# Kernel tuning notes

Measured on AMD Instinct MI355X. Metric: run time of the kernel, lower is better.

The kernel has to match this reference:

```python
import jax, jax.numpy as jnp
import numpy as np

N = 4096          # nodes (= Mamba sequence length)
E_EDGES = 65536   # edges
D = 512           # dim_h (= d_inner, expand=1)
NEXP = 4          # num_experts (cfg.model.num_experts)
DSTATE = 16
DCONV = 4
DTRANK = 32       # ceil(D/16)
EPS = 1e-5


def _silu(x):
    return x * jax.nn.sigmoid(x)


def _bn(h, g, b):
    # BatchNorm1d over node axis (batch statistics)
    mu = h.mean(0)
    var = h.var(0)
    return (h - mu) * jax.lax.rsqrt(var + EPS) * g + b


def _mamba(u, in_w, conv_w, conv_b, x_w, dt_w, dt_b, A_log, Dp, out_w):
    # u: [L, D] single-sequence Mamba(d_model=D, d_state=16, d_conv=4, expand=1)
    L = u.shape[0]
    xz = u @ in_w                      # [L, 2D]
    xc, z = xz[:, :D], xz[:, D:]
    xp = jnp.pad(xc, ((DCONV - 1, 0), (0, 0)))
    xconv = conv_b
    for k in range(DCONV):             # depthwise causal conv, tiny fixed loop
        xconv = xconv + conv_w[:, k] * xp[k:k + L]
    xs = _silu(xconv)                  # [L, D]
    dbc = xs @ x_w                     # [L, DTRANK + 2*DSTATE]
    dt = jax.nn.softplus(dbc[:, :DTRANK] @ dt_w + dt_b)          # [L, D]
    Bm = dbc[:, DTRANK:DTRANK + DSTATE]                          # [L, S]
    Cm = dbc[:, DTRANK + DSTATE:]                                # [L, S]
    A = -jnp.exp(A_log)                                          # [D, S]
    dA = jnp.exp(dt[:, :, None] * A[None])                       # [L, D, S]
    dBu = dt[:, :, None] * Bm[:, None, :] * xs[:, :, None]       # [L, D, S]

    def step(hprev, inp):
        dA_t, dBu_t, C_t = inp
        hn = dA_t * hprev + dBu_t
        return hn, (hn * C_t[None, :]).sum(-1)

    _, ys = jax.lax.scan(step, jnp.zeros((D, DSTATE), u.dtype), (dA, dBu, Cm))
    y = ys + Dp * xs
    return (y * _silu(z)) @ out_w      # [L, D]


def setup_inputs() -> dict:
    key = jax.random.key(0)
    ks = jax.random.split(key, 24)
    s = 1.0 / np.sqrt(D)
    inp = {}
    inp['x'] = jax.random.normal(ks[0], (N, D), jnp.float32)
    inp['edge_index'] = jax.random.randint(ks[1], (2, E_EDGES), 0, N)
    inp['edge_attr'] = jax.random.normal(ks[2], (E_EDGES, D), jnp.float32)
    # GINE nn: Linear(D,D) -> ReLU -> Linear(D,D)
    inp['gin_w1'] = jax.random.normal(ks[3], (D, D)) * s
    inp['gin_b1'] = jnp.zeros((D,))
    inp['gin_w2'] = jax.random.normal(ks[4], (D, D)) * s
    inp['gin_b2'] = jnp.zeros((D,))
    # BatchNorms
    inp['bn1l_g'] = jnp.ones((D,)); inp['bn1l_b'] = jnp.zeros((D,))
    inp['bn1a_g'] = jnp.ones((D,)); inp['bn1a_b'] = jnp.zeros((D,))
    inp['bn2_g'] = jnp.ones((D,)); inp['bn2_b'] = jnp.zeros((D,))
    # gating MLP [D, D//2, NEXP]
    inp['gate_w1'] = jax.random.normal(ks[5], (D, D // 2)) * s
    inp['gate_b1'] = jnp.zeros((D // 2,))
    inp['gate_w2'] = jax.random.normal(ks[6], (D // 2, NEXP)) * (1.0 / np.sqrt(D // 2))
    inp['gate_b2'] = jnp.zeros((NEXP,))
    # stacked per-expert Mamba params
    inp['in_w'] = jax.random.normal(ks[7], (NEXP, D, 2 * D)) * s
    inp['conv_w'] = jax.random.normal(ks[8], (NEXP, D, DCONV)) * 0.5
    inp['conv_b'] = jnp.zeros((NEXP, D))
    inp['x_w'] = jax.random.normal(ks[9], (NEXP, D, DTRANK + 2 * DSTATE)) * s
    inp['dt_w'] = jax.random.normal(ks[10], (NEXP, DTRANK, D)) * (1.0 / np.sqrt(DTRANK))
    inp['dt_b'] = jax.random.normal(ks[11], (NEXP, D)) * 0.1 - 4.0
    A0 = jnp.log(jnp.arange(1, DSTATE + 1, dtype=jnp.float32))
    inp['A_log'] = jnp.broadcast_to(A0, (NEXP, D, DSTATE)).copy()
    inp['Dp'] = jnp.ones((NEXP, D))
    inp['out_w'] = jax.random.normal(ks[12], (NEXP, D, D)) * s
    # FFN
    inp['ff_w1'] = jax.random.normal(ks[13], (D, 2 * D)) * s
    inp['ff_b1'] = jnp.zeros((2 * D,))
    inp['ff_w2'] = jax.random.normal(ks[14], (2 * D, D)) * (1.0 / np.sqrt(2 * D))
    inp['ff_b2'] = jnp.zeros((D,))
    return inp


def reference(x, edge_index, edge_attr,
              gin_w1, gin_b1, gin_w2, gin_b2,
              bn1l_g, bn1l_b, bn1a_g, bn1a_b, bn2_g, bn2_b,
              gate_w1, gate_b1, gate_w2, gate_b2,
              in_w, conv_w, conv_b, x_w, dt_w, dt_b, A_log, Dp, out_w,
              ff_w1, ff_b1, ff_w2, ff_b2):
    h_in = x
    src, dst = edge_index[0], edge_index[1]
    # local GINEConv: nn(x + sum_j relu(x_j + e_ji))
    msg = jax.nn.relu(x[src] + edge_attr)                      # [E, D]
    aggr = jax.ops.segment_sum(msg, dst, num_segments=N)       # [N, D]
    h_local = jax.nn.relu((x + aggr) @ gin_w1 + gin_b1) @ gin_w2 + gin_b2
    h_local = _bn(h_in + h_local, bn1l_g, bn1l_b)
    # gated mixture of Mamba experts
    gate = jax.nn.softmax(jax.nn.relu(x @ gate_w1 + gate_b1) @ gate_w2 + gate_b2, axis=-1)  # [N, NEXP]
    ys = jax.vmap(_mamba, in_axes=(None, 0, 0, 0, 0, 0, 0, 0, 0, 0))(
        x, in_w, conv_w, conv_b, x_w, dt_w, dt_b, A_log, Dp, out_w)  # [NEXP, N, D]
    h_attn = jnp.einsum('ne,end->nd', gate, ys)
    h_attn = _bn(h_in + h_attn, bn1a_g, bn1a_b)
    # fuse + FFN
    h = h_local + h_attn
    ff = jax.nn.relu(h @ ff_w1 + ff_b1) @ ff_w2 + ff_b2
    return _bn(h + ff, bn2_g, bn2_b)
```

## Files before the change

### kernel.cpp

```cpp
#include <hip/hip_runtime.h>
#include <hip/hip_bf16.h>
#include <math.h>

#define N_NODES 4096
#define E_EDGE 65536
#define D 512
#define NEXP 4
#define DSTATE 16
#define DCONV 4
#define DTRANK 32
#define EPS 1e-5f
#define LCHUNK 32
#define NCHUNK (N_NODES / LCHUNK)

typedef __hip_bfloat16 bf16;
typedef short bf16x8 __attribute__((ext_vector_type(8)));
typedef float f32x4 __attribute__((ext_vector_type(4)));

__device__ __forceinline__ float siluf(float x) { return x / (1.f + __expf(-x)); }
__device__ __forceinline__ float softplusf(float x) {
  return (x > 20.f) ? x : log1pf(__expf(x));
}

__device__ __forceinline__ void gload16(const void* g, void* l) {
  __builtin_amdgcn_global_load_lds(
      (const __attribute__((address_space(1))) void*)g,
      (__attribute__((address_space(3))) void*)l, 16, 0, 0);
}

template <int FN, int EPI>
__global__ __launch_bounds__(256, 2) void mm_k(
    const bf16* __restrict__ A, int lda, long sA,
    const bf16* __restrict__ Bt, int ldb, long sB,
    const float* __restrict__ bias,
    float* __restrict__ Cf, bf16* __restrict__ Cb, int ldc, long sC, int K) {
  constexpr int BN = FN * 32;
  __shared__ __align__(16) bf16 As[128 * 32];
  __shared__ __align__(16) bf16 Bs[BN * 32];
  const int z = blockIdx.z;
  A += (size_t)z * sA;
  Bt += (size_t)z * sB;
  const int tid = threadIdx.x;
  const int w = tid >> 6, l = tid & 63;
  const int wr = w >> 1, wc = w & 1;
  const int bm = blockIdx.y * 128, bn = blockIdx.x * BN;

  f32x4 acc[4][FN];
#pragma unroll
  for (int i = 0; i < 4; ++i)
#pragma unroll
    for (int j = 0; j < FN; ++j) acc[i][j] = 0.f;

  const int srow = l >> 2, schunk = l & 3;
  const bf16* gA = A + (size_t)(bm + w * 16 + srow) * lda + schunk * 8;
  const bf16* gB = Bt + (size_t)(bn + w * 16 + srow) * ldb + schunk * 8;
  bf16* lA = As + w * 512;
  bf16* lB = Bs + w * 512;

  const int ar = wr * 64 + (l & 15);
  const int br = wc * FN * 16 + (l & 15);
  const int kb = l >> 4;

  for (int k0 = 0; k0 < K; k0 += 32) {
    gload16(gA + k0, lA);
    gload16(gA + k0 + (size_t)64 * lda, lA + 64 * 32);
    gload16(gB + k0, lB);
    if (FN == 4) gload16(gB + k0 + (size_t)64 * ldb, lB + 64 * 32);
    __syncthreads();
    const bf16x8* Ap = (const bf16x8*)As;
    const bf16x8* Bp = (const bf16x8*)Bs;
    bf16x8 af[4], bfr[FN];
#pragma unroll
    for (int i = 0; i < 4; ++i) af[i] = Ap[(ar + i * 16) * 4 + kb];
#pragma unroll
    for (int j = 0; j < FN; ++j) bfr[j] = Bp[(br + j * 16) * 4 + kb];
#pragma unroll
    for (int i = 0; i < 4; ++i)
#pragma unroll
      for (int j = 0; j < FN; ++j)
        acc[i][j] = __builtin_amdgcn_mfma_f32_16x16x32_bf16(af[i], bfr[j], acc[i][j], 0, 0, 0);
    __syncthreads();
  }

  if (Cf) Cf += (size_t)z * sC;
  if (Cb) Cb += (size_t)z * sC;
  const int r0 = bm + wr * 64 + (l >> 4) * 4;
  const int c0 = bn + wc * FN * 16 + (l & 15);
#pragma unroll
  for (int i = 0; i < 4; ++i)
#pragma unroll
    for (int j = 0; j < FN; ++j) {
      const int col = c0 + j * 16;
      const float bv = bias ? bias[col] : 0.f;
#pragma unroll
      for (int r = 0; r < 4; ++r) {
        const int row = r0 + i * 16 + r;
        float v = acc[i][j][r] + bv;
        if (EPI == 1) v = fmaxf(v, 0.f);
        if (Cf) Cf[(size_t)row * ldc + col] = v;
        if (Cb) Cb[(size_t)row * ldc + col] = __float2bfloat16(v);
      }
    }
}

__global__ __launch_bounds__(256) void wtrans_k(const float* __restrict__ in,
                                                bf16* __restrict__ out, int K, int N,
                                                int ldo, long s_in, long s_out) {
  __shared__ float t[32][33];
  in += (size_t)blockIdx.z * s_in;
  out += (size_t)blockIdx.z * s_out;
  const int n0 = blockIdx.x * 32, k0 = blockIdx.y * 32;
  const int tx = threadIdx.x & 31, ty = threadIdx.x >> 5;
  for (int i = ty; i < 32; i += 8) t[i][tx] = in[(size_t)(k0 + i) * N + n0 + tx];
  __syncthreads();
  for (int i = ty; i < 32; i += 8)
    out[(size_t)(n0 + i) * ldo + k0 + tx] = __float2bfloat16(t[tx][i]);
}

__global__ void hist_k(const int* __restrict__ ei, int* __restrict__ deg) {
  int e = blockIdx.x * 256 + threadIdx.x;
  if (e < E_EDGE) atomicAdd(&deg[ei[E_EDGE + e]], 1);
}

__global__ __launch_bounds__(1024) void prefix_k(const int* __restrict__ deg,
                                                 int* __restrict__ rowstart) {
  __shared__ int s[1024];
  int t = threadIdx.x;
  int base = t * 4;
  int d0 = deg[base], d1 = deg[base + 1], d2 = deg[base + 2], d3 = deg[base + 3];
  int sum = d0 + d1 + d2 + d3;
  s[t] = sum;
  __syncthreads();
  for (int off = 1; off < 1024; off <<= 1) {
    int v = (t >= off) ? s[t - off] : 0;
    __syncthreads();
    s[t] += v;
    __syncthreads();
  }
  int excl = s[t] - sum;
  rowstart[base] = excl;
  rowstart[base + 1] = excl + d0;
  rowstart[base + 2] = excl + d0 + d1;
  rowstart[base + 3] = excl + d0 + d1 + d2;
}

__global__ void scatter_k(const int* __restrict__ ei, const int* __restrict__ rowstart,
                          int* __restrict__ cnt, int* __restrict__ eid) {
  int e = blockIdx.x * 256 + threadIdx.x;
  if (e < E_EDGE) {
    int dst = ei[E_EDGE + e];
    int slot = rowstart[dst] + atomicAdd(&cnt[dst], 1);
    eid[slot] = e;
  }
}

__global__ __launch_bounds__(256) void aggr_gather_k(
    const float* __restrict__ x, const int* __restrict__ ei, const float* __restrict__ ea,
    const int* __restrict__ rowstart, const int* __restrict__ deg,
    const int* __restrict__ eid, bf16* __restrict__ hpre, bf16* __restrict__ xbf) {
  int n = blockIdx.x;
  int tid = threadIdx.x;
  int beg = rowstart[n];
  int end = beg + deg[n];
  float a0 = 0.f, a1 = 0.f;
  int i = beg;
  for (; i + 1 < end; i += 2) {
    int e0 = eid[i], e1 = eid[i + 1];
    int s0 = ei[e0], s1 = ei[e1];
    const float* x0 = x + (size_t)s0 * D;
    const float* e0p = ea + (size_t)e0 * D;
    const float* x1 = x + (size_t)s1 * D;
    const float* e1p = ea + (size_t)e1 * D;
    a0 += fmaxf(x0[tid] + e0p[tid], 0.f) + fmaxf(x1[tid] + e1p[tid], 0.f);
    a1 += fmaxf(x0[tid + 256] + e0p[tid + 256], 0.f) +
          fmaxf(x1[tid + 256] + e1p[tid + 256], 0.f);
  }
  if (i < end) {
    int e0 = eid[i];
    int s0 = ei[e0];
    const float* x0 = x + (size_t)s0 * D;
    const float* e0p = ea + (size_t)e0 * D;
    a0 += fmaxf(x0[tid] + e0p[tid], 0.f);
    a1 += fmaxf(x0[tid + 256] + e0p[tid + 256], 0.f);
  }
  float xv0 = x[(size_t)n * D + tid];
  float xv1 = x[(size_t)n * D + tid + 256];
  hpre[(size_t)n * D + tid] = __float2bfloat16(xv0 + a0);
  hpre[(size_t)n * D + tid + 256] = __float2bfloat16(xv1 + a1);
  xbf[(size_t)n * D + tid] = __float2bfloat16(xv0);
  xbf[(size_t)n * D + tid + 256] = __float2bfloat16(xv1);
}

__global__ __launch_bounds__(256) void gate2_k(const float* __restrict__ g1,
                                               const float* __restrict__ w2,
                                               const float* __restrict__ b2,
                                               float* __restrict__ gate) {
  int row = blockIdx.x * 4 + (threadIdx.x >> 6);
  int lane = threadIdx.x & 63;
  float a0 = 0.f, a1 = 0.f, a2 = 0.f, a3 = 0.f;
  for (int k = lane; k < 256; k += 64) {
    float v = g1[(size_t)row * 256 + k];
    a0 = fmaf(v, w2[k * 4 + 0], a0);
    a1 = fmaf(v, w2[k * 4 + 1], a1);
    a2 = fmaf(v, w2[k * 4 + 2], a2);
    a3 = fmaf(v, w2[k * 4 + 3], a3);
  }
#pragma unroll
  for (int off = 32; off; off >>= 1) {
    a0 += __shfl_down(a0, off);
    a1 += __shfl_down(a1, off);
    a2 += __shfl_down(a2, off);
    a3 += __shfl_down(a3, off);
  }
  if (lane == 0) {
    float l0 = a0 + b2[0], l1 = a1 + b2[1], l2 = a2 + b2[2], l3 = a3 + b2[3];
    float m = fmaxf(fmaxf(l0, l1), fmaxf(l2, l3));
    float e0 = __expf(l0 - m), e1 = __expf(l1 - m), e2 = __expf(l2 - m), e3 = __expf(l3 - m);
    float s = 1.f / (e0 + e1 + e2 + e3);
    gate[row * 4 + 0] = e0 * s;
    gate[row * 4 + 1] = e1 * s;
    gate[row * 4 + 2] = e2 * s;
    gate[row * 4 + 3] = e3 * s;
  }
}

__global__ void conv_silu_k(const bf16* __restrict__ xz, const float* __restrict__ cw,
                            const float* __restrict__ cb, bf16* __restrict__ xs, int e0) {
  const int z = blockIdx.y;
  xz += (size_t)z * N_NODES * 2 * D;
  xs += (size_t)z * N_NODES * D;
  cw += (size_t)(e0 + z) * D * DCONV;
  cb += (size_t)(e0 + z) * D;
  int idx = blockIdx.x * blockDim.x + threadIdx.x;
  if (idx >= N_NODES * D) return;
  int t = idx >> 9;
  int d = idx & (D - 1);
  float acc = cb[d];
#pragma unroll
  for (int k = 0; k < DCONV; ++k) {
    int tt = t + k - (DCONV - 1);
    if (tt >= 0)
      acc = fmaf(cw[d * DCONV + k], __bfloat162float(xz[(size_t)tt * (2 * D) + d]), acc);
  }
  xs[idx] = __float2bfloat16(siluf(acc));
}

__global__ void dt_k(const float* __restrict__ dbc, const float* __restrict__ dtw,
                     const float* __restrict__ dtbias, bf16* __restrict__ dt, int e0) {
  const int z = blockIdx.y;
  dbc += (size_t)z * N_NODES * 64;
  dt += (size_t)z * N_NODES * D;
  dtw += (size_t)(e0 + z) * DTRANK * D;
  dtbias += (size_t)(e0 + z) * D;
  int idx = blockIdx.x * blockDim.x + threadIdx.x;
  int t = idx >> 9, d = idx & (D - 1);
  float acc = dtbias[d];
#pragma unroll
  for (int k = 0; k < DTRANK; ++k) acc = fmaf(dbc[t * 64 + k], dtw[k * D + d], acc);
  dt[idx] = __float2bfloat16(softplusf(acc));
}

__global__ __launch_bounds__(256) void colstats_k(const float* __restrict__ p,
                                                  const float* __restrict__ q,
                                                  float* __restrict__ acc) {
  __shared__ float sb[4][512], sb2[4][512];
  const int w = threadIdx.x >> 6, l = threadIdx.x & 63;
  float s[8], s2[8];
#pragma unroll
  for (int i = 0; i < 8; ++i) { s[i] = 0.f; s2[i] = 0.f; }
  for (int j = 0; j < 16; ++j) {
    size_t base = ((size_t)blockIdx.x * 64 + w * 16 + j) * D;
#pragma unroll
    for (int i = 0; i < 8; ++i) {
      int c = i * 64 + l;
      float v = p[base + c] + q[base + c];
      s[i] += v;
      s2[i] = fmaf(v, v, s2[i]);
    }
  }
#pragma unroll
  for (int i = 0; i < 8; ++i) {
    sb[w][i * 64 + l] = s[i];
    sb2[w][i * 64 + l] = s2[i];
  }
  __syncthreads();
  for (int c = threadIdx.x; c < 512; c += 256) {
    atomicAdd(&acc[c], sb[0][c] + sb[1][c] + sb[2][c] + sb[3][c]);
    atomicAdd(&acc[512 + c], sb2[0][c] + sb2[1][c] + sb2[2][c] + sb2[3][c]);
  }
}

__device__ __forceinline__ void bn_params(const float* acc, int d, float& mu, float& rsig) {
  mu = acc[d] * (1.f / N_NODES);
  float var = acc[512 + d] * (1.f / N_NODES) - mu * mu;
  rsig = rsqrtf(var + EPS);
}

__global__ void norm_k(const float* __restrict__ p, const float* __restrict__ q,
                       const float* __restrict__ acc, const float* __restrict__ g,
                       const float* __restrict__ b, float* __restrict__ o) {
  int idx = blockIdx.x * blockDim.x + threadIdx.x;
  if (idx >= N_NODES * D) return;
  int d = idx & (D - 1);
  float mu, rsig;
  bn_params(acc, d, mu, rsig);
  o[idx] = (p[idx] + q[idx] - mu) * rsig * g[d] + b[d];
}

__global__ void bnadd_k(const float* __restrict__ x, const float* __restrict__ hraw,
                        const float* __restrict__ acc, const float* __restrict__ g,
                        const float* __restrict__ b, const float* __restrict__ hloc,
                        float* __restrict__ of, bf16* __restrict__ ob) {
  int idx = blockIdx.x * blockDim.x + threadIdx.x;
  if (idx >= N_NODES * D) return;
  int d = idx & (D - 1);
  float mu, rsig;
  bn_params(acc, d, mu, rsig);
  float v = hloc[idx] + (x[idx] + hraw[idx] - mu) * rsig * g[d] + b[d];
  of[idx] = v;
  ob[idx] = __float2bfloat16(v);
}

__global__ __launch_bounds__(512) void scanA_k(const bf16* __restrict__ dt,
                                               const bf16* __restrict__ xs,
                                               const float* __restrict__ dbc,
                                               const float* __restrict__ Alog,
                                               float* __restrict__ Q,
                                               float* __restrict__ dtsum, int e0) {
  const int z = blockIdx.y;
  dt += (size_t)z * N_NODES * D;
  xs += (size_t)z * N_NODES * D;
  dbc += (size_t)z * N_NODES * 64;
  Alog += (size_t)(e0 + z) * D * DSTATE;
  Q += (size_t)z * NCHUNK * D * DSTATE;
  dtsum += (size_t)z * NCHUNK * D;
  int c = blockIdx.x;
  int d = threadIdx.x;
  float As[DSTATE], h[DSTATE];
#pragma unroll
  for (int s = 0; s < DSTATE; ++s) {
    As[s] = -__expf(Alog[d * DSTATE + s]);
    h[s] = 0.f;
  }
  float dts = 0.f;
  int t0 = c * LCHUNK;
  for (int t = t0; t < t0 + LCHUNK; ++t) {
    float dtv = __bfloat162float(dt[(size_t)t * D + d]);
    float xv = __bfloat162float(xs[(size_t)t * D + d]);
    float bx = dtv * xv;
    dts += dtv;
#pragma unroll
    for (int s = 0; s < DSTATE; ++s) {
      float Bv = dbc[(size_t)t * 64 + DTRANK + s];
      h[s] = fmaf(__expf(dtv * As[s]), h[s], bx * Bv);
    }
  }
  size_t base = ((size_t)c * D + d) * DSTATE;
#pragma unroll
  for (int s = 0; s < DSTATE; ++s) Q[base + s] = h[s];
  dtsum[c * D + d] = dts;
}

__global__ __launch_bounds__(256) void scanB_k(const float* __restrict__ Q,
                                               const float* __restrict__ dtsum,
                                               const float* __restrict__ Alog,
                                               float* __restrict__ Hin, int e0) {
  const int z = blockIdx.y;
  Q += (size_t)z * NCHUNK * D * DSTATE;
  dtsum += (size_t)z * NCHUNK * D;
  Alog += (size_t)(e0 + z) * D * DSTATE;
  Hin += (size_t)z * NCHUNK * D * DSTATE;
  int idx = blockIdx.x * blockDim.x + threadIdx.x;
  int d = idx >> 4;
  float As = -__expf(Alog[idx]);
  float h = 0.f;
  for (int c = 0; c < NCHUNK; ++c) {
    size_t base = (size_t)c * D * DSTATE + idx;
    Hin[base] = h;
    h = fmaf(__expf(As * dtsum[c * D + d]), h, Q[base]);
  }
}

__global__ __launch_bounds__(512) void scanC_k(const bf16* __restrict__ dt,
                                               const bf16* __restrict__ xs,
                                               const float* __restrict__ dbc,
                                               const float* __restrict__ Alog,
                                               const float* __restrict__ Hin,
                                               const bf16* __restrict__ xz,
                                               const float* __restrict__ Dp,
                                               const float* __restrict__ gate,
                                               bf16* __restrict__ u, int e0) {
  const int z = blockIdx.y;
  dt += (size_t)z * N_NODES * D;
  xs += (size_t)z * N_NODES * D;
  dbc += (size_t)z * N_NODES * 64;
  Alog += (size_t)(e0 + z) * D * DSTATE;
  Hin += (size_t)z * NCHUNK * D * DSTATE;
  xz += (size_t)z * N_NODES * 2 * D;
  Dp += (size_t)(e0 + z) * D;
  u += (size_t)(e0 + z) * 512;
  const int ge = e0 + z;
  int c = blockIdx.x;
  int d = threadIdx.x;
  float As[DSTATE], h[DSTATE];
  size_t base = ((size_t)c * D + d) * DSTATE;
#pragma unroll
  for (int s = 0; s < DSTATE; ++s) {
    As[s] = -__expf(Alog[d * DSTATE + s]);
    h[s] = Hin[base + s];
  }
  float Dv = Dp[d];
  int t0 = c * LCHUNK;
  for (int t = t0; t < t0 + LCHUNK; ++t) {
    float dtv = __bfloat162float(dt[(size_t)t * D + d]);
    float xv = __bfloat162float(xs[(size_t)t * D + d]);
    float bx = dtv * xv;
    float y = 0.f;
#pragma unroll
    for (int s = 0; s < DSTATE; ++s) {
      float Bv = dbc[(size_t)t * 64 + DTRANK + s];
      float Cv = dbc[(size_t)t * 64 + DTRANK + DSTATE + s];
      h[s] = fmaf(__expf(dtv * As[s]), h[s], bx * Bv);
      y = fmaf(h[s], Cv, y);
    }
    float zv = __bfloat162float(xz[(size_t)t * (2 * D) + D + d]);
    float gv = gate[t * NEXP + ge];
    u[(size_t)t * 2048 + d] = __float2bfloat16(gv * (y + Dv * xv) * siluf(zv));
  }
}

extern "C" void kernel_launch(void* const* d_in, const int* in_sizes, int n_in,
                              void* d_out, int out_size, void* d_ws, size_t ws_size,
                              hipStream_t stream) {
  const float* x = (const float*)d_in[0];
  const int* ei = (const int*)d_in[1];
  const float* ea = (const float*)d_in[2];
  const float* gin_w1 = (const float*)d_in[3];
  const float* gin_b1 = (const float*)d_in[4];
  const float* gin_w2 = (const float*)d_in[5];
  const float* gin_b2 = (const float*)d_in[6];
  const float* bn1l_g = (const float*)d_in[7];
  const float* bn1l_b = (const float*)d_in[8];
  const float* bn1a_g = (const float*)d_in[9];
  const float* bn1a_b = (const float*)d_in[10];
  const float* bn2_g = (const float*)d_in[11];
  const float* bn2_b = (const float*)d_in[12];
  const float* gate_w1 = (const float*)d_in[13];
  const float* gate_b1 = (const float*)d_in[14];
  const float* gate_w2 = (const float*)d_in[15];
  const float* gate_b2 = (const float*)d_in[16];
  const float* in_w = (const float*)d_in[17];
  const float* conv_w = (const float*)d_in[18];
  const float* conv_b = (const float*)d_in[19];
  const float* x_w = (const float*)d_in[20];
  const float* dt_w = (const float*)d_in[21];
  const float* dt_b = (const float*)d_in[22];
  const float* A_log = (const float*)d_in[23];
  const float* Dp = (const float*)d_in[24];
  const float* out_w = (const float*)d_in[25];
  const float* ff_w1 = (const float*)d_in[26];
  const float* ff_b1 = (const float*)d_in[27];
  const float* ff_w2 = (const float*)d_in[28];
  const float* ff_b2 = (const float*)d_in[29];
  float* out = (float*)d_out;

  const size_t ND = (size_t)N_NODES * D;
  const size_t NDb = ND / 2;

  const size_t fixed_f = 3 * ND + (size_t)N_NODES * 256 + 16384 + 2490624 + ND + 2048 +
                         81920 + 2 * ND + 4096;
  const size_t per_f = 2 * ND + NDb + (size_t)N_NODES * 64 + NDb +
                       2 * (size_t)NCHUNK * D * DSTATE + (size_t)NCHUNK * D;
  const int EB = (ws_size >= (fixed_f + 4 * per_f + 65536) * sizeof(float)) ? 4 : 1;

  float* ws = (float*)d_ws;
  size_t off = 0;
  auto alloc = [&](size_t n) {
    float* p = ws + off;
    off += (n + 63) & ~(size_t)63;
    return p;
  };
  float* ffo = alloc(ND);
  float* pbuf = alloc(ND);
  float* hlocal = alloc(ND);
  float* g1 = alloc((size_t)N_NODES * 256);
  float* gate = alloc((size_t)N_NODES * NEXP);
  bf16* gw1t = (bf16*)alloc(131072);
  bf16* gw2t = (bf16*)alloc(131072);
  bf16* gatew1t = (bf16*)alloc(65536);
  bf16* inwt = (bf16*)alloc(1048576);
  bf16* xwt = (bf16*)alloc(65536);
  bf16* outwt_cat = (bf16*)alloc(524288);
  bf16* ffw1t = (bf16*)alloc(262144);
  bf16* ffw2t = (bf16*)alloc(262144);
  int* deg = (int*)alloc(N_NODES);
  int* cnt = (int*)alloc(N_NODES);
  float* accs = alloc(3072);
  int* eid = (int*)alloc(E_EDGE);
  int* rowstart = (int*)alloc(N_NODES);
  float* xbf_f = alloc(NDb);
  float* xz_f = alloc((size_t)EB * ND);
  float* xs_f = alloc((size_t)EB * NDb);
  float* dbc = alloc((size_t)EB * N_NODES * 64);
  float* dtb_f = alloc((size_t)EB * NDb);
  float* Qb = alloc((size_t)EB * NCHUNK * D * DSTATE);
  float* Hin = alloc((size_t)EB * NCHUNK * D * DSTATE);
  float* dtsum = alloc((size_t)EB * NCHUNK * D);
  float* ucat_f = alloc(4 * NDb);
  float* hattn_raw = alloc(ND);
  float* acc1 = accs, *acc2 = accs + 1024, *acc3 = accs + 2048;

  bf16* x_bf = (bf16*)xbf_f;
  bf16* hpre_bf = (bf16*)pbuf;
  bf16* t1_bf = (bf16*)(pbuf + NDb);
  bf16* xz_bf = (bf16*)xz_f;
  bf16* xs_bf = (bf16*)xs_f;
  bf16* dt_bf = (bf16*)dtb_f;
  bf16* ucat = (bf16*)ucat_f;
  float* hcomb = xz_f;
  bf16* hcomb_bf = (bf16*)(ucat_f);
  bf16* ffh_bf = (bf16*)pbuf;

  const int nelem = N_NODES * D;
  const int ew = (nelem + 255) / 256;

  hipMemsetAsync(deg, 0, (N_NODES + N_NODES + 3072) * sizeof(float), stream);

  wtrans_k<<<dim3(16, 16, 1), 256, 0, stream>>>(gin_w1, gw1t, 512, 512, 512, 0, 0);
  wtrans_k<<<dim3(16, 16, 1), 256, 0, stream>>>(gin_w2, gw2t, 512, 512, 512, 0, 0);
  wtrans_k<<<dim3(8, 16, 1), 256, 0, stream>>>(gate_w1, gatew1t, 512, 256, 512, 0, 0);
  wtrans_k<<<dim3(32, 16, 4), 256, 0, stream>>>(in_w, inwt, 512, 1024, 512,
                                                (long)512 * 1024, (long)512 * 1024);
  wtrans_k<<<dim3(2, 16, 4), 256, 0, stream>>>(x_w, xwt, 512, 64, 512, (long)512 * 64,
                                               (long)64 * 512);
  wtrans_k<<<dim3(16, 16, 4), 256, 0, stream>>>(out_w, outwt_cat, 512, 512, 2048,
                                                (long)512 * 512, (long)512);
  wtrans_k<<<dim3(32, 16, 1), 256, 0, stream>>>(ff_w1, ffw1t, 512, 1024, 512, 0, 0);
  wtrans_k<<<dim3(16, 32, 1), 256, 0, stream>>>(ff_w2, ffw2t, 1024, 512, 1024, 0, 0);

  hist_k<<<E_EDGE / 256, 256, 0, stream>>>(ei, deg);
  prefix_k<<<1, 1024, 0, stream>>>(deg, rowstart);
  scatter_k<<<E_EDGE / 256, 256, 0, stream>>>(ei, rowstart, cnt, eid);
  aggr_gather_k<<<N_NODES, 256, 0, stream>>>(x, ei, ea, rowstart, deg, eid, hpre_bf, x_bf);
  mm_k<2, 1><<<dim3(8, 32, 1), 256, 0, stream>>>(hpre_bf, 512, 0, gw1t, 512, 0, gin_b1,
                                                 nullptr, t1_bf, 512, 0, 512);
  mm_k<2, 0><<<dim3(8, 32, 1), 256, 0, stream>>>(t1_bf, 512, 0, gw2t, 512, 0, gin_b2,
                                                 hlocal, nullptr, 512, 0, 512);
  colstats_k<<<64, 256, 0, stream>>>(x, hlocal, acc1);
  norm_k<<<ew, 256, 0, stream>>>(x, hlocal, acc1, bn1l_g, bn1l_b, hlocal);

  mm_k<2, 1><<<dim3(4, 32, 1), 256, 0, stream>>>(x_bf, 512, 0, gatew1t, 512, 0, gate_b1,
                                                 g1, nullptr, 256, 0, 512);
  gate2_k<<<N_NODES / 4, 256, 0, stream>>>(g1, gate_w2, gate_b2, gate);

  for (int e0 = 0; e0 < NEXP; e0 += EB) {
    mm_k<4, 0><<<dim3(8, 32, EB), 256, 0, stream>>>(
        x_bf, 512, 0, inwt + (size_t)e0 * 512 * 1024, 512, (long)512 * 1024, nullptr,
        nullptr, xz_bf, 1024, (long)N_NODES * 1024, 512);
    conv_silu_k<<<dim3(ew, EB), 256, 0, stream>>>(xz_bf, conv_w, conv_b, xs_bf, e0);
    mm_k<2, 0><<<dim3(1, 32, EB), 256, 0, stream>>>(
        xs_bf, 512, (long)ND, xwt + (size_t)e0 * 64 * 512, 512, (long)64 * 512, nullptr,
        dbc, nullptr, 64, (long)N_NODES * 64, 512);
    dt_k<<<dim3(ew, EB), 256, 0, stream>>>(dbc, dt_w, dt_b, dt_bf, e0);
    scanA_k<<<dim3(NCHUNK, EB), 512, 0, stream>>>(dt_bf, xs_bf, dbc, A_log, Qb, dtsum, e0);
    scanB_k<<<dim3((D * DSTATE) / 256, EB), 256, 0, stream>>>(Qb, dtsum, A_log, Hin, e0);
    scanC_k<<<dim3(NCHUNK, EB), 512, 0, stream>>>(dt_bf, xs_bf, dbc, A_log, Hin, xz_bf, Dp,
                                                  gate, ucat, e0);
  }
  mm_k<2, 0><<<dim3(8, 32, 1), 256, 0, stream>>>(ucat, 2048, 0, outwt_cat, 2048, 0,
                                                 nullptr, hattn_raw, nullptr, 512, 0, 2048);

  colstats_k<<<64, 256, 0, stream>>>(x, hattn_raw, acc2);
  bnadd_k<<<ew, 256, 0, stream>>>(x, hattn_raw, acc2, bn1a_g, bn1a_b, hlocal, hcomb,
                                  hcomb_bf);
  mm_k<4, 1><<<dim3(8, 32, 1), 256, 0, stream>>>(hcomb_bf, 512, 0, ffw1t, 512, 0, ff_b1,
                                                 nullptr, ffh_bf, 1024, 0, 512);
  mm_k<2, 0><<<dim3(8, 32, 1), 256, 0, stream>>>(ffh_bf, 1024, 0, ffw2t, 1024, 0, ff_b2,
                                                 ffo, nullptr, 512, 0, 1024);
  colstats_k<<<64, 256, 0, stream>>>(hcomb, ffo, acc3);
  norm_k<<<ew, 256, 0, stream>>>(hcomb, ffo, acc3, bn2_g, bn2_b, out);
}
```

Baseline: 493.9 us.

## Vectorize GEMM epilogue, batch weight transposes, fuse both batchnorm passes

The GEMM kernel swaps the MFMA operand order so each lane holds four consecutive output columns, which lets the epilogue write with vector f32x4 and bf16x4 stores instead of scalar ones. The eight weight-transpose launches become a single launch that looks up its work from a table of per-matrix offsets. The separate colstats and normalize passes for the local branch are merged with the attention-branch ones into one dual-statistics kernel and one combined normalize-add kernel, so fewer launches run and the full-size tensors are read fewer times. In exchange, the fused stats kernel holds more registers, and the table lookup adds a small search in every transpose block.

Result: faster. 460.0 us (-6.9%).

```diff
diff --git a/kernel.cpp b/kernel.cpp
--- a/kernel.cpp
+++ b/kernel.cpp
@@ -16,10 +16,15 @@
 typedef __hip_bfloat16 bf16;
 typedef short bf16x8 __attribute__((ext_vector_type(8)));
 typedef float f32x4 __attribute__((ext_vector_type(4)));
+typedef unsigned short u16x4 __attribute__((ext_vector_type(4)));
 
 __device__ __forceinline__ float siluf(float x) { return x / (1.f + __expf(-x)); }
 __device__ __forceinline__ float softplusf(float x) {
   return (x > 20.f) ? x : log1pf(__expf(x));
+}
+__device__ __forceinline__ unsigned short f2bf(float v) {
+  bf16 b = __float2bfloat16(v);
+  return *reinterpret_cast<unsigned short*>(&b);
 }
 
 __device__ __forceinline__ void gload16(const void* g, void* l) {
@@ -78,43 +83,65 @@
     for (int i = 0; i < 4; ++i)
 #pragma unroll
       for (int j = 0; j < FN; ++j)
-        acc[i][j] = __builtin_amdgcn_mfma_f32_16x16x32_bf16(af[i], bfr[j], acc[i][j], 0, 0, 0);
+        acc[i][j] = __builtin_amdgcn_mfma_f32_16x16x32_bf16(bfr[j], af[i], acc[i][j], 0, 0, 0);
     __syncthreads();
   }
 
   if (Cf) Cf += (size_t)z * sC;
   if (Cb) Cb += (size_t)z * sC;
-  const int r0 = bm + wr * 64 + (l >> 4) * 4;
-  const int c0 = bn + wc * FN * 16 + (l & 15);
-#pragma unroll
-  for (int i = 0; i < 4; ++i)
+  const int r0 = bm + wr * 64 + (l & 15);
+  const int cb0 = bn + wc * FN * 16 + ((l >> 4) << 2);
+#pragma unroll
+  for (int i = 0; i < 4; ++i) {
+    const int row = r0 + i * 16;
 #pragma unroll
     for (int j = 0; j < FN; ++j) {
-      const int col = c0 + j * 16;
-      const float bv = bias ? bias[col] : 0.f;
-#pragma unroll
-      for (int r = 0; r < 4; ++r) {
-        const int row = r0 + i * 16 + r;
-        float v = acc[i][j][r] + bv;
-        if (EPI == 1) v = fmaxf(v, 0.f);
-        if (Cf) Cf[(size_t)row * ldc + col] = v;
-        if (Cb) Cb[(size_t)row * ldc + col] = __float2bfloat16(v);
+      const int col = cb0 + j * 16;
+      f32x4 v = acc[i][j];
+      if (bias) v += *(const f32x4*)&bias[col];
+      if (EPI == 1) {
+#pragma unroll
+        for (int r = 0; r < 4; ++r) v[r] = fmaxf(v[r], 0.f);
+      }
+      if (Cf) *(f32x4*)&Cf[(size_t)row * ldc + col] = v;
+      if (Cb) {
+        u16x4 u;
+#pragma unroll
+        for (int r = 0; r < 4; ++r) u[r] = f2bf(v[r]);
+        *(u16x4*)&Cb[(size_t)row * ldc + col] = u;
       }
     }
-}
-
-__global__ __launch_bounds__(256) void wtrans_k(const float* __restrict__ in,
-                                                bf16* __restrict__ out, int K, int N,
-                                                int ldo, long s_in, long s_out) {
+  }
+}
+
+struct WtArgs {
+  const float* in[8];
+  bf16* out[8];
+  int K[8], N[8], ldo[8];
+  long sin[8], sout[8];
+  int cum[8];
+};
+__global__ __launch_bounds__(256) void wtrans_all_k(WtArgs a) {
   __shared__ float t[32][33];
-  in += (size_t)blockIdx.z * s_in;
-  out += (size_t)blockIdx.z * s_out;
-  const int n0 = blockIdx.x * 32, k0 = blockIdx.y * 32;
+  int b = blockIdx.x;
+  int i = 0;
+  while (b >= a.cum[i]) ++i;
+  int local = b - (i ? a.cum[i - 1] : 0);
+  const int ntx = a.N[i] / 32;
+  const int nty = a.K[i] / 32;
+  const int perz = ntx * nty;
+  const int z = local / perz;
+  const int rem = local - z * perz;
+  const int bx = rem % ntx, by = rem / ntx;
+  const float* in = a.in[i] + (size_t)z * a.sin[i];
+  bf16* out = a.out[i] + (size_t)z * a.sout[i];
+  const int N = a.N[i], ldo = a.ldo[i];
+  const int n0 = bx * 32, k0 = by * 32;
   const int tx = threadIdx.x & 31, ty = threadIdx.x >> 5;
-  for (int i = ty; i < 32; i += 8) t[i][tx] = in[(size_t)(k0 + i) * N + n0 + tx];
+  for (int r = ty; r < 32; r += 8) t[r][tx] = in[(size_t)(k0 + r) * N + n0 + tx];
   __syncthreads();
-  for (int i = ty; i < 32; i += 8)
-    out[(size_t)(n0 + i) * ldo + k0 + tx] = __float2bfloat16(t[tx][i]);
+  for (int r = ty; r < 32; r += 8)
+    out[(size_t)(n0 + r) * ldo + k0 + tx] = __float2bfloat16(t[tx][r]);
 }
 
 __global__ void hist_k(const int* __restrict__ ei, int* __restrict__ deg) {
@@ -290,6 +317,53 @@
   }
 }
 
+__global__ __launch_bounds__(256) void colstats2_k(const float* __restrict__ x,
+                                                   const float* __restrict__ p,
+                                                   const float* __restrict__ q,
+                                                   float* __restrict__ acc1,
+                                                   float* __restrict__ acc2) {
+  __shared__ float sb[4][512], sb2[4][512];
+  const int w = threadIdx.x >> 6, l = threadIdx.x & 63;
+  float s1[8], s1q[8], s2[8], s2q[8];
+#pragma unroll
+  for (int i = 0; i < 8; ++i) { s1[i] = 0.f; s1q[i] = 0.f; s2[i] = 0.f; s2q[i] = 0.f; }
+  for (int j = 0; j < 16; ++j) {
+    size_t base = ((size_t)blockIdx.x * 64 + w * 16 + j) * D;
+#pragma unroll
+    for (int i = 0; i < 8; ++i) {
+      int c = i * 64 + l;
+      float xv = x[base + c];
+      float v1 = xv + p[base + c];
+      float v2 = xv + q[base + c];
+      s1[i] += v1;
+      s1q[i] = fmaf(v1, v1, s1q[i]);
+      s2[i] += v2;
+      s2q[i] = fmaf(v2, v2, s2q[i]);
+    }
+  }
+#pragma unroll
+  for (int i = 0; i < 8; ++i) {
+    sb[w][i * 64 + l] = s1[i];
+    sb2[w][i * 64 + l] = s1q[i];
+  }
+  __syncthreads();
+  for (int c = threadIdx.x; c < 512; c += 256) {
+    atomicAdd(&acc1[c], sb[0][c] + sb[1][c] + sb[2][c] + sb[3][c]);
+    atomicAdd(&acc1[512 + c], sb2[0][c] + sb2[1][c] + sb2[2][c] + sb2[3][c]);
+  }
+  __syncthreads();
+#pragma unroll
+  for (int i = 0; i < 8; ++i) {
+    sb[w][i * 64 + l] = s2[i];
+    sb2[w][i * 64 + l] = s2q[i];
+  }
+  __syncthreads();
+  for (int c = threadIdx.x; c < 512; c += 256) {
+    atomicAdd(&acc2[c], sb[0][c] + sb[1][c] + sb[2][c] + sb[3][c]);
+    atomicAdd(&acc2[512 + c], sb2[0][c] + sb2[1][c] + sb2[2][c] + sb2[3][c]);
+  }
+}
+
 __device__ __forceinline__ void bn_params(const float* acc, int d, float& mu, float& rsig) {
   mu = acc[d] * (1.f / N_NODES);
   float var = acc[512 + d] * (1.f / N_NODES) - mu * mu;
@@ -307,16 +381,21 @@
   o[idx] = (p[idx] + q[idx] - mu) * rsig * g[d] + b[d];
 }
 
-__global__ void bnadd_k(const float* __restrict__ x, const float* __restrict__ hraw,
-                        const float* __restrict__ acc, const float* __restrict__ g,
-                        const float* __restrict__ b, const float* __restrict__ hloc,
-                        float* __restrict__ of, bf16* __restrict__ ob) {
+__global__ void bnadd2_k(const float* __restrict__ x, const float* __restrict__ hloc,
+                         const float* __restrict__ hattn, const float* __restrict__ acc1,
+                         const float* __restrict__ acc2, const float* __restrict__ g1,
+                         const float* __restrict__ b1, const float* __restrict__ g2,
+                         const float* __restrict__ b2, float* __restrict__ of,
+                         bf16* __restrict__ ob) {
   int idx = blockIdx.x * blockDim.x + threadIdx.x;
   if (idx >= N_NODES * D) return;
   int d = idx & (D - 1);
-  float mu, rsig;
-  bn_params(acc, d, mu, rsig);
-  float v = hloc[idx] + (x[idx] + hraw[idx] - mu) * rsig * g[d] + b[d];
+  float mu1, rs1, mu2, rs2;
+  bn_params(acc1, d, mu1, rs1);
+  bn_params(acc2, d, mu2, rs2);
+  float xv = x[idx];
+  float v = (xv + hloc[idx] - mu1) * rs1 * g1[d] + b1[d] +
+            (xv + hattn[idx] - mu2) * rs2 * g2[d] + b2[d];
   of[idx] = v;
   ob[idx] = __float2bfloat16(v);
 }
@@ -526,17 +605,28 @@
 
   hipMemsetAsync(deg, 0, (N_NODES + N_NODES + 3072) * sizeof(float), stream);
 
-  wtrans_k<<<dim3(16, 16, 1), 256, 0, stream>>>(gin_w1, gw1t, 512, 512, 512, 0, 0);
-  wtrans_k<<<dim3(16, 16, 1), 256, 0, stream>>>(gin_w2, gw2t, 512, 512, 512, 0, 0);
-  wtrans_k<<<dim3(8, 16, 1), 256, 0, stream>>>(gate_w1, gatew1t, 512, 256, 512, 0, 0);
-  wtrans_k<<<dim3(32, 16, 4), 256, 0, stream>>>(in_w, inwt, 512, 1024, 512,
-                                                (long)512 * 1024, (long)512 * 1024);
-  wtrans_k<<<dim3(2, 16, 4), 256, 0, stream>>>(x_w, xwt, 512, 64, 512, (long)512 * 64,
-                                               (long)64 * 512);
-  wtrans_k<<<dim3(16, 16, 4), 256, 0, stream>>>(out_w, outwt_cat, 512, 512, 2048,
-                                                (long)512 * 512, (long)512);
-  wtrans_k<<<dim3(32, 16, 1), 256, 0, stream>>>(ff_w1, ffw1t, 512, 1024, 512, 0, 0);
-  wtrans_k<<<dim3(16, 32, 1), 256, 0, stream>>>(ff_w2, ffw2t, 1024, 512, 1024, 0, 0);
+  WtArgs wa;
+  const float* wsrc[8] = {gin_w1, gin_w2, gate_w1, in_w, x_w, out_w, ff_w1, ff_w2};
+  bf16* wdst[8] = {gw1t, gw2t, gatew1t, inwt, xwt, outwt_cat, ffw1t, ffw2t};
+  int wK[8] = {512, 512, 512, 512, 512, 512, 512, 1024};
+  int wN[8] = {512, 512, 256, 1024, 64, 512, 1024, 512};
+  int wldo[8] = {512, 512, 512, 512, 512, 2048, 512, 1024};
+  long wsin[8] = {0, 0, 0, (long)512 * 1024, (long)512 * 64, (long)512 * 512, 0, 0};
+  long wsout[8] = {0, 0, 0, (long)512 * 1024, (long)64 * 512, 512, 0, 0};
+  int wz[8] = {1, 1, 1, 4, 4, 4, 1, 1};
+  int cum = 0;
+  for (int i = 0; i < 8; ++i) {
+    wa.in[i] = wsrc[i];
+    wa.out[i] = wdst[i];
+    wa.K[i] = wK[i];
+    wa.N[i] = wN[i];
+    wa.ldo[i] = wldo[i];
+    wa.sin[i] = wsin[i];
+    wa.sout[i] = wsout[i];
+    cum += (wN[i] / 32) * (wK[i] / 32) * wz[i];
+    wa.cum[i] = cum;
+  }
+  wtrans_all_k<<<cum, 256, 0, stream>>>(wa);
 
   hist_k<<<E_EDGE / 256, 256, 0, stream>>>(ei, deg);
   prefix_k<<<1, 1024, 0, stream>>>(deg, rowstart);
@@ -546,8 +636,6 @@
                                                  nullptr, t1_bf, 512, 0, 512);
   mm_k<2, 0><<<dim3(8, 32, 1), 256, 0, stream>>>(t1_bf, 512, 0, gw2t, 512, 0, gin_b2,
                                                  hlocal, nullptr, 512, 0, 512);
-  colstats_k<<<64, 256, 0, stream>>>(x, hlocal, acc1);
-  norm_k<<<ew, 256, 0, stream>>>(x, hlocal, acc1, bn1l_g, bn1l_b, hlocal);
 
   mm_k<2, 1><<<dim3(4, 32, 1), 256, 0, stream>>>(x_bf, 512, 0, gatew1t, 512, 0, gate_b1,
                                                  g1, nullptr, 256, 0, 512);
@@ -570,9 +658,9 @@
   mm_k<2, 0><<<dim3(8, 32, 1), 256, 0, stream>>>(ucat, 2048, 0, outwt_cat, 2048, 0,
                                                  nullptr, hattn_raw, nullptr, 512, 0, 2048);
 
-  colstats_k<<<64, 256, 0, stream>>>(x, hattn_raw, acc2);
-  bnadd_k<<<ew, 256, 0, stream>>>(x, hattn_raw, acc2, bn1a_g, bn1a_b, hlocal, hcomb,
-                                  hcomb_bf);
+  colstats2_k<<<64, 256, 0, stream>>>(x, hlocal, hattn_raw, acc1, acc2);
+  bnadd2_k<<<ew, 256, 0, stream>>>(x, hlocal, hattn_raw, acc1, acc2, bn1l_g, bn1l_b,
+                                   bn1a_g, bn1a_b, hcomb, hcomb_bf);
   mm_k<4, 1><<<dim3(8, 32, 1), 256, 0, stream>>>(hcomb_bf, 512, 0, ffw1t, 512, 0, ff_b1,
                                                  nullptr, ffh_bf, 1024, 0, 512);
   mm_k<2, 0><<<dim3(8, 32, 1), 256, 0, stream>>>(ffh_bf, 1024, 0, ffw2t, 1024, 0, ff_b2,
```
